# Optimization experiments

Hardware: AMD Instinct MI355X
Metric: run time of the kernel (lower is better)

## Reference

```python
import jax, jax.numpy as jnp
import numpy as np

V, D, OUT, H, FF, L, K, POOL = 4097, 128, 64, 8, 256, 2, 9, 20
B, LE, LP = 32, 3000, 2000
GRID, WIDTH = 5, 257
DR = OUT // 8  # channel-attention reduction


def _ln(x, p):
    mu = jnp.mean(x, -1, keepdims=True)
    var = jnp.mean((x - mu) ** 2, -1, keepdims=True)
    return (x - mu) * jax.lax.rsqrt(var + 1e-5) * p[0] + p[1]


def _rope(x):
    # x: [B,H,S,hd], interleaved rotary embedding
    S, hd = x.shape[-2], x.shape[-1]
    inv = 1.0 / (10000.0 ** (jnp.arange(0, hd, 2, dtype=jnp.float32) / hd))
    ang = jnp.arange(S, dtype=jnp.float32)[:, None] * inv[None, :]  # [S,hd/2]
    c, s = jnp.cos(ang), jnp.sin(ang)
    x1, x2 = x[..., 0::2], x[..., 1::2]
    return jnp.stack([x1 * c - x2 * s, x1 * s + x2 * c], axis=-1).reshape(x.shape)


def _cbat_layer(x, qkv_w, qkv_b, o_w, o_b, ca_w1, ca_w2, sa_w,
                ff1_w, ff1_b, ff2_w, ff2_b, ln1, ln2):
    # x: [B,S,d] (batch-first inside CBAT, matching x.permute(1,0,2) in torch)
    Bx, S, d = x.shape
    hd = d // H

    def proj(i):
        return (x @ qkv_w[i] + qkv_b[i]).reshape(Bx, S, H, hd).transpose(0, 2, 1, 3)

    q, k, v = proj(0), proj(1), proj(2)
    q, k = _rope(q), _rope(k)
    attn = jax.nn.softmax(jnp.einsum('bhqd,bhkd->bhqk', q, k) / jnp.sqrt(jnp.float32(hd)), axis=-1)
    ctx = jnp.einsum('bhqk,bhkd->bhqd', attn, v).transpose(0, 2, 1, 3).reshape(Bx, S, d)
    # CBAM-style channel attention (pool over sequence)
    avg, mx = ctx.mean(1), ctx.max(1)  # [B,d]
    ca = jax.nn.sigmoid(jax.nn.relu(avg @ ca_w1) @ ca_w2 + jax.nn.relu(mx @ ca_w1) @ ca_w2)
    ctx = ctx * ca[:, None, :]
    # CBAM-style spatial attention (pool over channels, conv over sequence)
    feat = jnp.stack([ctx.mean(-1), ctx.max(-1)], axis=1)  # [B,2,S]
    sa = jax.nn.sigmoid(jax.lax.conv_general_dilated(
        feat, sa_w[None], (1,), 'SAME', dimension_numbers=('NCH', 'OIH', 'NCH')))  # [B,1,S]
    ctx = ctx * sa.transpose(0, 2, 1)
    out = ctx @ o_w + o_b
    aloss = jnp.mean(attn ** 2)  # adaptive attention regularizer
    x = _ln(x + out, ln1)
    ff = jax.nn.relu(x @ ff1_w + ff1_b) @ ff2_w + ff2_b
    x = _ln(x + ff, ln2)
    return x, aloss


def _mha(q_in, k_in, v_in, in_w, in_b, out_w, out_b):
    # torch nn.MultiheadAttention math (batch-first layout here; math identical)
    d = q_in.shape[-1]
    hd = d // H
    Wq, Wk, Wv = jnp.split(in_w, 3, 0)
    bq, bk, bv = jnp.split(in_b, 3, 0)

    def heads(t):
        return t.reshape(t.shape[0], t.shape[1], H, hd).transpose(0, 2, 1, 3)

    q, k, v = heads(q_in @ Wq.T + bq), heads(k_in @ Wk.T + bk), heads(v_in @ Wv.T + bv)
    attn = jax.nn.softmax(jnp.einsum('bhqd,bhkd->bhqk', q, k) / jnp.sqrt(jnp.float32(hd)), axis=-1)
    ctx = jnp.einsum('bhqk,bhkd->bhqd', attn, v).transpose(0, 2, 1, 3).reshape(q_in.shape)
    return ctx @ out_w.T + out_b


def _fourier(x, wc, ws, b):
    # FourierKAN layer: sum_k a*cos(kx) + b*sin(kx)
    kx = x[:, :, None] * jnp.arange(1, GRID + 1, dtype=x.dtype)  # [B,in,g]
    return jnp.einsum('big,oig->bo', jnp.cos(kx), wc) + jnp.einsum('big,oig->bo', jnp.sin(kx), ws) + b


def _frontend(ids, emb, conv_w, conv_b, bn):
    x = emb[ids]  # [B,Lseq,D]
    x = jax.lax.conv_general_dilated(x.transpose(0, 2, 1), conv_w, (1,), 'VALID',
                                     dimension_numbers=('NCH', 'OIH', 'NCH')) + conv_b[None, :, None]
    x = jax.nn.relu(x)
    x = jax.lax.reduce_window(x, -jnp.inf, jax.lax.max, (1, 1, POOL), (1, 1, POOL), 'VALID')
    g, be, mu, var = bn[0], bn[1], bn[2], bn[3]  # BatchNorm1d (eval mode)
    x = (x - mu[None, :, None]) * jax.lax.rsqrt(var[None, :, None] + 1e-5) * g[None, :, None] + be[None, :, None]
    return x.transpose(0, 2, 1)  # [B,S,OUT]


def _forward(enhancer_ids, promoter_ids, emb_en, emb_pr, conv_w_en, conv_b_en, conv_w_pr, conv_b_pr,
             bn_en, bn_pr, t_qkv_w, t_qkv_b, t_o_w, t_o_b, t_ca_w1, t_ca_w2, t_sa_w,
             t_ff1_w, t_ff1_b, t_ff2_w, t_ff2_b, t_ln1, t_ln2,
             cross_in_w, cross_in_b, cross_out_w, cross_out_b,
             self_in_w, self_in_b, self_out_w, self_out_b,
             fk1_c, fk1_s, fk1_b, fk2_c, fk2_s, fk2_b):
    en = _frontend(enhancer_ids, emb_en, conv_w_en, conv_b_en, bn_en)
    pr = _frontend(promoter_ids, emb_pr, conv_w_pr, conv_b_pr, bn_pr)
    total_aloss = jnp.float32(0.0)
    branches = [en, pr]
    for s in range(2):  # 0=enhancer stack, 1=promoter stack
        x = branches[s]
        for l in range(L):
            x, al = _cbat_layer(x, t_qkv_w[s, l], t_qkv_b[s, l], t_o_w[s, l], t_o_b[s, l],
                                t_ca_w1[s, l], t_ca_w2[s, l], t_sa_w[s, l],
                                t_ff1_w[s, l], t_ff1_b[s, l], t_ff2_w[s, l], t_ff2_b[s, l],
                                t_ln1[s, l], t_ln2[s, l])
            total_aloss = total_aloss + al
        branches[s] = x
    en, pr = branches
    en_att = _mha(en, pr, pr, cross_in_w, cross_in_b, cross_out_w, cross_out_b)
    en_fin = _mha(en_att, en_att, en_att, self_in_w, self_in_b, self_out_w, self_out_b)
    pr_fin = _mha(pr, pr, pr, self_in_w, self_in_b, self_out_w, self_out_b)
    combined = jnp.concatenate([en_fin.mean(1), pr_fin.mean(1)], axis=1)  # AdaptiveAvgPool1d(1)
    hidden = _fourier(combined, fk1_c, fk1_s, fk1_b)
    result = _fourier(hidden, fk2_c, fk2_s, fk2_b)
    return jax.nn.sigmoid(result), combined, total_aloss


def setup_inputs() -> dict:
    key = jax.random.key(0)
    ks = iter(jax.random.split(key, 64))

    def nrm(shape, sc=0.02):
        return jax.random.normal(next(ks), shape, jnp.float32) * sc

    ln_init = lambda: jnp.stack([jnp.ones((2, L, OUT)), jnp.zeros((2, L, OUT))], axis=2)
    inp = {
        'enhancer_ids': jax.random.randint(next(ks), (B, LE), 0, V),
        'promoter_ids': jax.random.randint(next(ks), (B, LP), 0, V),
        'enhancer_features': jax.random.normal(next(ks), (B, 10), jnp.float32),
        'promoter_features': jax.random.normal(next(ks), (B, 10), jnp.float32),
        'emb_en': nrm((V, D), 0.1), 'emb_pr': nrm((V, D), 0.1),
        'conv_w_en': nrm((OUT, D, K)), 'conv_b_en': jnp.zeros((OUT,)),
        'conv_w_pr': nrm((OUT, D, K)), 'conv_b_pr': jnp.zeros((OUT,)),
        'bn_en': jnp.stack([jnp.ones(OUT), jnp.zeros(OUT), jnp.zeros(OUT), jnp.ones(OUT)]),
        'bn_pr': jnp.stack([jnp.ones(OUT), jnp.zeros(OUT), jnp.zeros(OUT), jnp.ones(OUT)]),
        't_qkv_w': nrm((2, L, 3, OUT, OUT)), 't_qkv_b': jnp.zeros((2, L, 3, OUT)),
        't_o_w': nrm((2, L, OUT, OUT)), 't_o_b': jnp.zeros((2, L, OUT)),
        't_ca_w1': nrm((2, L, OUT, DR)), 't_ca_w2': nrm((2, L, DR, OUT)),
        't_sa_w': nrm((2, L, 2, 7)),
        't_ff1_w': nrm((2, L, OUT, FF)), 't_ff1_b': jnp.zeros((2, L, FF)),
        't_ff2_w': nrm((2, L, FF, OUT)), 't_ff2_b': jnp.zeros((2, L, OUT)),
        't_ln1': ln_init(), 't_ln2': ln_init(),
        'cross_in_w': nrm((3 * OUT, OUT)), 'cross_in_b': jnp.zeros((3 * OUT,)),
        'cross_out_w': nrm((OUT, OUT)), 'cross_out_b': jnp.zeros((OUT,)),
        'self_in_w': nrm((3 * OUT, OUT)), 'self_in_b': jnp.zeros((3 * OUT,)),
        'self_out_w': nrm((OUT, OUT)), 'self_out_b': jnp.zeros((OUT,)),
        'fk1_c': nrm((WIDTH, 2 * OUT, GRID), 0.1), 'fk1_s': nrm((WIDTH, 2 * OUT, GRID), 0.1),
        'fk1_b': jnp.zeros((WIDTH,)),
        'fk2_c': nrm((1, WIDTH, GRID), 0.1), 'fk2_s': nrm((1, WIDTH, GRID), 0.1),
        'fk2_b': jnp.zeros((1,)),
    }
    return inp


def reference(enhancer_ids, promoter_ids, enhancer_features, promoter_features,
              emb_en, emb_pr, conv_w_en, conv_b_en, conv_w_pr, conv_b_pr,
              bn_en, bn_pr, t_qkv_w, t_qkv_b, t_o_w, t_o_b, t_ca_w1, t_ca_w2, t_sa_w,
              t_ff1_w, t_ff1_b, t_ff2_w, t_ff2_b, t_ln1, t_ln2,
              cross_in_w, cross_in_b, cross_out_w, cross_out_b,
              self_in_w, self_in_b, self_out_w, self_out_b,
              fk1_c, fk1_s, fk1_b, fk2_c, fk2_s, fk2_b):
    # enhancer_features / promoter_features are accepted but unused by the original forward
    return _forward(enhancer_ids, promoter_ids, emb_en, emb_pr, conv_w_en, conv_b_en,
                    conv_w_pr, conv_b_pr, bn_en, bn_pr, t_qkv_w, t_qkv_b, t_o_w, t_o_b,
                    t_ca_w1, t_ca_w2, t_sa_w, t_ff1_w, t_ff1_b, t_ff2_w, t_ff2_b, t_ln1, t_ln2,
                    cross_in_w, cross_in_b, cross_out_w, cross_out_b,
                    self_in_w, self_in_b, self_out_w, self_out_b,
                    fk1_c, fk1_s, fk1_b, fk2_c, fk2_s, fk2_b)
```

## Files before the change

kernel.cpp:

```cpp
#include <hip/hip_runtime.h>
#include <math.h>

#define BB 32
#define SE 149
#define SP 99
#define LE_LEN 3000
#define LP_LEN 2000
#define VT 8
#define ROWS_EN (BB * SE)
#define ROWS_PR (BB * SP)
#define ROWS_ALL (ROWS_EN + ROWS_PR)

__device__ __forceinline__ void row_decode(int row, int& branch, int& b,
                                           int& s, int& S, int& lrow) {
  if (row < ROWS_EN) { branch = 0; S = SE; lrow = row; b = row / SE; s = row - b * SE; }
  else { branch = 1; S = SP; lrow = row - ROWS_EN; b = lrow / SP; s = lrow - b * SP; }
}

__global__ __launch_bounds__(256) void prep_kernel(
    const float* __restrict__ cw_en, const float* __restrict__ cw_pr,
    const float* __restrict__ cross_in, const float* __restrict__ cross_out,
    const float* __restrict__ self_in, const float* __restrict__ self_out,
    float* __restrict__ W2en, float* __restrict__ W2pr,
    float* __restrict__ Wt, float* __restrict__ Al) {
  int bb = blockIdx.x;
  if (bb == 0 && threadIdx.x == 0) Al[0] = 0.f;
  if (bb < 576) {
    const float* src = (bb < 288) ? cw_en : cw_pr;
    float* dst = (bb < 288) ? W2en : W2pr;
    int i = ((bb < 288) ? bb : bb - 288) * 256 + threadIdx.x;
    int oc = i / 1152, r = i % 1152, ic = r / 9, k = r % 9;
    dst[ic * 576 + k * 64 + oc] = src[i];
  } else {
    int m = bb - 576;
    const float* src = (m < 3) ? cross_in + m * 4096
                     : (m == 3) ? cross_out
                     : (m < 7) ? self_in + (m - 4) * 4096
                     : self_out;
    for (int i = threadIdx.x; i < 4096; i += 256) {
      int o = i >> 6, c = i & 63;
      Wt[m * 4096 + c * 64 + o] = src[i];
    }
  }
}

__global__ __launch_bounds__(192) void conv_table_kernel(
    const float* __restrict__ emb_en, const float* __restrict__ emb_pr,
    const float* __restrict__ W2en, const float* __restrict__ W2pr,
    float* __restrict__ Cen, float* __restrict__ Cpr) {
  int blk = blockIdx.x;
  int branch = (blk >= 513);
  const float* emb = branch ? emb_pr : emb_en;
  const float* W2 = branch ? W2pr : W2en;
  float* C = branch ? Cpr : Cen;
  int v0 = (branch ? blk - 513 : blk) * VT;
  __shared__ float e[VT][128];
  int t = threadIdx.x;
  int nv = 4097 - v0; if (nv > VT) nv = VT;
  for (int i = t; i < nv * 128; i += 192) e[i >> 7][i & 127] = emb[v0 * 128 + i];
  __syncthreads();
  float a0[VT], a1[VT], a2[VT];
#pragma unroll
  for (int v = 0; v < VT; ++v) { a0[v] = 0.f; a1[v] = 0.f; a2[v] = 0.f; }
  for (int ic = 0; ic < 128; ++ic) {
    float w0 = W2[ic * 576 + t];
    float w1 = W2[ic * 576 + t + 192];
    float w2 = W2[ic * 576 + t + 384];
#pragma unroll
    for (int v = 0; v < VT; ++v) {
      float ev = e[v][ic];
      a0[v] += ev * w0; a1[v] += ev * w1; a2[v] += ev * w2;
    }
  }
  for (int v = 0; v < nv; ++v) {
    C[(size_t)(v0 + v) * 576 + t] = a0[v];
    C[(size_t)(v0 + v) * 576 + t + 192] = a1[v];
    C[(size_t)(v0 + v) * 576 + t + 384] = a2[v];
  }
}

__global__ __launch_bounds__(256) void frontend_kernel(
    const int* __restrict__ en_ids, const int* __restrict__ pr_ids,
    const float* __restrict__ Cen, const float* __restrict__ Cpr,
    const float* __restrict__ cb_en, const float* __restrict__ cb_pr,
    const float* __restrict__ bn_en, const float* __restrict__ bn_pr,
    float* __restrict__ Xen, float* __restrict__ Xpr) {
  int t = threadIdx.x;
  int wid = t >> 6, oc = t & 63;
  int row = blockIdx.x * 4 + wid;
  int branch, b, s, S, lrow;
  row_decode(row, branch, b, s, S, lrow);
  const int* ids = branch ? pr_ids : en_ids;
  int Lin = branch ? LP_LEN : LE_LEN;
  const float* C = branch ? Cpr : Cen;
  const float* cb = branch ? cb_pr : cb_en;
  const float* bn = branch ? bn_pr : bn_en;
  float* X = branch ? Xpr : Xen;
  __shared__ int idl[4][28];
  if (oc < 28) idl[wid][oc] = ids[b * Lin + s * 20 + oc];
  __syncthreads();
  float bias = cb[oc];
  float m = -INFINITY;
  for (int p = 0; p < 20; ++p) {
    float acc = bias;
#pragma unroll
    for (int k = 0; k < 9; ++k) acc += C[idl[wid][p + k] * 576 + k * 64 + oc];
    acc = fmaxf(acc, 0.f);
    m = fmaxf(m, acc);
  }
  float g = bn[oc], be = bn[64 + oc], mu = bn[128 + oc], var = bn[192 + oc];
  X[(size_t)lrow * 64 + oc] = (m - mu) * rsqrtf(var + 1e-5f) * g + be;
}

__global__ __launch_bounds__(256) void qkv_rope_kernel(
    const float* __restrict__ Xen, const float* __restrict__ Xpr,
    const float* __restrict__ t_qkv_w, const float* __restrict__ t_qkv_b, int l,
    float* __restrict__ Q, float* __restrict__ K, float* __restrict__ V) {
  int t = threadIdx.x;
  int wid = t >> 6, oc = t & 63;
  int row = blockIdx.x * 4 + wid;
  int branch, b, s, S, lrow;
  row_decode(row, branch, b, s, S, lrow);
  const float* X = branch ? Xpr : Xen;
  int idx = branch * 2 + l;
  const float* W = t_qkv_w + (size_t)idx * 3 * 4096;
  const float* bias = t_qkv_b + idx * 192;
  __shared__ float xr[4][64], qs[4][64], ks[4][64];
  xr[wid][oc] = X[lrow * 64 + oc];
  __syncthreads();
  float q0 = bias[oc], k0 = bias[64 + oc], v0 = bias[128 + oc];
  float q1 = 0.f, k1 = 0.f, v1 = 0.f;
  for (int c = 0; c < 64; c += 2) {
    float xa = xr[wid][c], xb = xr[wid][c + 1];
    q0 += xa * W[c * 64 + oc];
    q1 += xb * W[(c + 1) * 64 + oc];
    k0 += xa * W[4096 + c * 64 + oc];
    k1 += xb * W[4096 + (c + 1) * 64 + oc];
    v0 += xa * W[8192 + c * 64 + oc];
    v1 += xb * W[8192 + (c + 1) * 64 + oc];
  }
  float q = q0 + q1, k = k0 + k1, v = v0 + v1;
  qs[wid][oc] = q; ks[wid][oc] = k;
  V[row * 64 + oc] = v;
  __syncthreads();
  int j = oc & 7;
  int p = j >> 1;
  float inv = powf(10000.f, -(float)p * 0.25f);
  float ang = (float)s * inv;
  float cc = cosf(ang), ss = sinf(ang);
  float qo, ko;
  if ((j & 1) == 0) {
    qo = qs[wid][oc] * cc - qs[wid][oc + 1] * ss;
    ko = ks[wid][oc] * cc - ks[wid][oc + 1] * ss;
  } else {
    qo = qs[wid][oc - 1] * ss + qs[wid][oc] * cc;
    ko = ks[wid][oc - 1] * ss + ks[wid][oc] * cc;
  }
  Q[row * 64 + oc] = qo;
  K[row * 64 + oc] = ko;
}

__global__ __launch_bounds__(256) void attn_kernel(
    const float* __restrict__ Q, const float* __restrict__ K,
    const float* __restrict__ V, float* __restrict__ ctx,
    int nblk0, int Sq0, int Sk0, int qb0, int kb0, float als0,
    int Sq1, int Sk1, int qb1, int kb1, float als1,
    float* __restrict__ aloss_acc) {
  int blk = blockIdx.x;
  int bh, Sq, Sk, qb, kb; float als;
  if (blk < nblk0) { bh = blk; Sq = Sq0; Sk = Sk0; qb = qb0; kb = kb0; als = als0; }
  else { bh = blk - nblk0; Sq = Sq1; Sk = Sk1; qb = qb1; kb = kb1; als = als1; }
  int b = bh >> 3, h = bh & 7;
  __shared__ float kk[160 * 8], vv[160 * 8];
  int t = threadIdx.x;
  for (int i = t; i < Sk * 8; i += 256) {
    int r = i >> 3, j = i & 7;
    kk[i] = K[(kb + b * Sk + r) * 64 + h * 8 + j];
    vv[i] = V[(kb + b * Sk + r) * 64 + h * 8 + j];
  }
  __syncthreads();
  float rowsum2 = 0.f;
  if (t < Sq) {
    float q[8];
#pragma unroll
    for (int j = 0; j < 8; ++j) q[j] = Q[(qb + b * Sq + t) * 64 + h * 8 + j];
    float m = -INFINITY, sum = 0.f, sum2 = 0.f, acc[8];
#pragma unroll
    for (int j = 0; j < 8; ++j) acc[j] = 0.f;
    const float sc = 0.35355339059327373f;
    for (int kki = 0; kki < Sk; ++kki) {
      float sdot = 0.f;
#pragma unroll
      for (int j = 0; j < 8; ++j) sdot += q[j] * kk[kki * 8 + j];
      sdot *= sc;
      if (sdot > m) {
        float f = expf(m - sdot);
        sum *= f; sum2 *= f * f;
#pragma unroll
        for (int j = 0; j < 8; ++j) acc[j] *= f;
        m = sdot;
      }
      float e = expf(sdot - m);
      sum += e; sum2 += e * e;
#pragma unroll
      for (int j = 0; j < 8; ++j) acc[j] += e * vv[kki * 8 + j];
    }
    float invs = 1.f / sum;
#pragma unroll
    for (int j = 0; j < 8; ++j)
      ctx[(qb + b * Sq + t) * 64 + h * 8 + j] = acc[j] * invs;
    rowsum2 = sum2 * invs * invs;
  }
  if (als != 0.f) {
    float wsum = rowsum2;
    for (int off = 32; off; off >>= 1) wsum += __shfl_down(wsum, off, 64);
    __shared__ float wred[4];
    if ((t & 63) == 0) wred[t >> 6] = wsum;
    __syncthreads();
    if (t == 0) {
      float tot = wred[0] + wred[1] + wred[2] + wred[3];
      atomicAdd(aloss_acc, tot * als);
    }
  }
}

__global__ __launch_bounds__(512) void ca_kernel(
    const float* __restrict__ ctx, const float* __restrict__ t_ca_w1,
    const float* __restrict__ t_ca_w2, int l, float* __restrict__ ca) {
  int bp = blockIdx.x;
  int branch = bp >> 5, b = bp & 31;
  int S = branch ? SP : SE;
  int base = branch ? ROWS_EN : 0;
  int idx = branch * 2 + l;
  const float* W1 = t_ca_w1 + idx * 512;
  const float* W2 = t_ca_w2 + idx * 512;
  int t = threadIdx.x;
  int c = t & 63, seg = t >> 6;
  float sum = 0.f, mx = -INFINITY;
  for (int s = seg; s < S; s += 8) {
    float v = ctx[(size_t)(base + b * S + s) * 64 + c];
    sum += v; mx = fmaxf(mx, v);
  }
  __shared__ float ssum[8][64], smx[8][64];
  ssum[seg][c] = sum; smx[seg][c] = mx;
  __syncthreads();
  __shared__ float avg_l[64], mx_l[64], ha[8], hm[8];
  if (t < 64) {
    float a = 0.f, m = -INFINITY;
#pragma unroll
    for (int g = 0; g < 8; ++g) { a += ssum[g][t]; m = fmaxf(m, smx[g][t]); }
    avg_l[t] = a / (float)S; mx_l[t] = m;
  }
  __syncthreads();
  if (t < 8) {
    float a = 0.f, m2 = 0.f;
    for (int i = 0; i < 64; ++i) {
      a += avg_l[i] * W1[i * 8 + t];
      m2 += mx_l[i] * W1[i * 8 + t];
    }
    ha[t] = fmaxf(a, 0.f); hm[t] = fmaxf(m2, 0.f);
  }
  __syncthreads();
  if (t < 64) {
    float o = 0.f;
#pragma unroll
    for (int j = 0; j < 8; ++j) o += (ha[j] + hm[j]) * W2[j * 64 + t];
    ca[bp * 64 + t] = 1.f / (1.f + expf(-o));
  }
}

__global__ __launch_bounds__(256) void feat_kernel(
    float* __restrict__ ctx, const float* __restrict__ ca,
    float* __restrict__ fmean, float* __restrict__ fmax) {
  int row = blockIdx.x * 4 + (threadIdx.x >> 6);
  int branch, b, s, S, lrow;
  row_decode(row, branch, b, s, S, lrow);
  int c = threadIdx.x & 63;
  float v = ctx[row * 64 + c] * ca[(branch * 32 + b) * 64 + c];
  ctx[row * 64 + c] = v;
  float sum = v, mx = v;
  for (int off = 32; off; off >>= 1) {
    sum += __shfl_xor(sum, off, 64);
    mx = fmaxf(mx, __shfl_xor(mx, off, 64));
  }
  if (c == 0) { fmean[row] = sum * (1.f / 64.f); fmax[row] = mx; }
}

__global__ __launch_bounds__(256) void tail_kernel(
    const float* __restrict__ ctx, const float* __restrict__ fmean,
    const float* __restrict__ fmax, const float* __restrict__ t_sa_w,
    const float* __restrict__ t_o_w, const float* __restrict__ t_o_b,
    const float* __restrict__ t_ln1, const float* __restrict__ t_ff1_w,
    const float* __restrict__ t_ff1_b, const float* __restrict__ t_ff2_w,
    const float* __restrict__ t_ff2_b, const float* __restrict__ t_ln2,
    int l, float* __restrict__ Xen, float* __restrict__ Xpr) {
  int t = threadIdx.x;
  int wid = t >> 6, lane = t & 63;
  int row = blockIdx.x * 4 + wid;
  int branch, b, s, S, lrow;
  row_decode(row, branch, b, s, S, lrow);
  int idx = branch * 2 + l;
  const float* sa_w = t_sa_w + idx * 14;
  float sa = 0.f;
  if (lane == 0) {
    for (int k = 0; k < 7; ++k) {
      int p = s + k - 3;
      if (p >= 0 && p < S)
        sa += fmean[row - s + p] * sa_w[k] + fmax[row - s + p] * sa_w[7 + k];
    }
    sa = 1.f / (1.f + expf(-sa));
  }
  sa = __shfl(sa, 0, 64);
  __shared__ float rowv[4][64], xr[4][64], h[4][256];
  rowv[wid][lane] = ctx[row * 64 + lane] * sa;
  __syncthreads();
  const float* o_w = t_o_w + (size_t)idx * 4096;
  float p0 = t_o_b[idx * 64 + lane], p1 = 0.f, p2 = 0.f, p3 = 0.f;
  for (int c = 0; c < 64; c += 4) {
    p0 += rowv[wid][c] * o_w[c * 64 + lane];
    p1 += rowv[wid][c + 1] * o_w[(c + 1) * 64 + lane];
    p2 += rowv[wid][c + 2] * o_w[(c + 2) * 64 + lane];
    p3 += rowv[wid][c + 3] * o_w[(c + 3) * 64 + lane];
  }
  float o = (p0 + p1) + (p2 + p3);
  float* X = branch ? Xpr : Xen;
  float r = X[lrow * 64 + lane] + o;
  float mu = r;
  for (int of = 32; of; of >>= 1) mu += __shfl_xor(mu, of, 64);
  mu *= (1.f / 64.f);
  float d = r - mu;
  float var = d * d;
  for (int of = 32; of; of >>= 1) var += __shfl_xor(var, of, 64);
  var *= (1.f / 64.f);
  const float* ln1 = t_ln1 + idx * 128;
  float x1 = d * rsqrtf(var + 1e-5f) * ln1[lane] + ln1[64 + lane];
  xr[wid][lane] = x1;
  __syncthreads();
  const float* W1 = t_ff1_w + (size_t)idx * 16384;
  float a0 = t_ff1_b[idx * 256 + t], a1 = a0, a2 = a0, a3 = a0;
  for (int c = 0; c < 64; ++c) {
    float w = W1[c * 256 + t];
    a0 += xr[0][c] * w; a1 += xr[1][c] * w; a2 += xr[2][c] * w; a3 += xr[3][c] * w;
  }
  h[0][t] = fmaxf(a0, 0.f); h[1][t] = fmaxf(a1, 0.f);
  h[2][t] = fmaxf(a2, 0.f); h[3][t] = fmaxf(a3, 0.f);
  __syncthreads();
  const float* W2 = t_ff2_w + (size_t)idx * 16384;
  float q0 = t_ff2_b[idx * 64 + lane], q1 = 0.f, q2 = 0.f, q3 = 0.f;
  for (int j = 0; j < 256; j += 4) {
    q0 += h[wid][j] * W2[j * 64 + lane];
    q1 += h[wid][j + 1] * W2[(j + 1) * 64 + lane];
    q2 += h[wid][j + 2] * W2[(j + 2) * 64 + lane];
    q3 += h[wid][j + 3] * W2[(j + 3) * 64 + lane];
  }
  float o2 = (q0 + q1) + (q2 + q3);
  float r2 = x1 + o2;
  mu = r2;
  for (int of = 32; of; of >>= 1) mu += __shfl_xor(mu, of, 64);
  mu *= (1.f / 64.f);
  d = r2 - mu;
  var = d * d;
  for (int of = 32; of; of >>= 1) var += __shfl_xor(var, of, 64);
  var *= (1.f / 64.f);
  const float* ln2 = t_ln2 + idx * 128;
  X[lrow * 64 + lane] = d * rsqrtf(var + 1e-5f) * ln2[lane] + ln2[64 + lane];
}

__global__ __launch_bounds__(256) void cross_proj_kernel(
    const float* __restrict__ Xen, const float* __restrict__ Xpr,
    const float* __restrict__ Wt, const float* __restrict__ bias,
    float* __restrict__ Q, float* __restrict__ K, float* __restrict__ V) {
  int t = threadIdx.x;
  int wid = t >> 6, oc = t & 63;
  int blk = blockIdx.x;
  __shared__ float xr[4][64];
  if (blk < ROWS_EN / 4) {
    int row = blk * 4 + wid;
    xr[wid][oc] = Xen[row * 64 + oc];
    __syncthreads();
    float p0 = bias[oc], p1 = 0.f, p2 = 0.f, p3 = 0.f;
    for (int c = 0; c < 64; c += 4) {
      p0 += xr[wid][c] * Wt[c * 64 + oc];
      p1 += xr[wid][c + 1] * Wt[(c + 1) * 64 + oc];
      p2 += xr[wid][c + 2] * Wt[(c + 2) * 64 + oc];
      p3 += xr[wid][c + 3] * Wt[(c + 3) * 64 + oc];
    }
    Q[row * 64 + oc] = (p0 + p1) + (p2 + p3);
  } else {
    int lr = (blk - ROWS_EN / 4) * 4 + wid;
    xr[wid][oc] = Xpr[lr * 64 + oc];
    __syncthreads();
    float k0 = bias[64 + oc], k1 = 0.f, v0 = bias[128 + oc], v1 = 0.f;
    for (int c = 0; c < 64; c += 2) {
      float xa = xr[wid][c], xb = xr[wid][c + 1];
      k0 += xa * Wt[4096 + c * 64 + oc];
      k1 += xb * Wt[4096 + (c + 1) * 64 + oc];
      v0 += xa * Wt[8192 + c * 64 + oc];
      v1 += xb * Wt[8192 + (c + 1) * 64 + oc];
    }
    K[(ROWS_EN + lr) * 64 + oc] = k0 + k1;
    V[(ROWS_EN + lr) * 64 + oc] = v0 + v1;
  }
}

__global__ __launch_bounds__(256) void self_qkv_kernel(
    const float* __restrict__ inEn, const float* __restrict__ inPr,
    const float* __restrict__ Wt, const float* __restrict__ bias,
    float* __restrict__ Q, float* __restrict__ K, float* __restrict__ V) {
  int t = threadIdx.x;
  int wid = t >> 6, oc = t & 63;
  int row = blockIdx.x * 4 + wid;
  const float* in; int lrow;
  if (row < ROWS_EN) { in = inEn; lrow = row; }
  else { in = inPr; lrow = row - ROWS_EN; }
  __shared__ float xr[4][64];
  xr[wid][oc] = in[lrow * 64 + oc];
  __syncthreads();
  float q0 = bias[oc], k0 = bias[64 + oc], v0 = bias[128 + oc];
  float q1 = 0.f, k1 = 0.f, v1 = 0.f;
  for (int c = 0; c < 64; c += 2) {
    float xa = xr[wid][c], xb = xr[wid][c + 1];
    q0 += xa * Wt[c * 64 + oc];
    q1 += xb * Wt[(c + 1) * 64 + oc];
    k0 += xa * Wt[4096 + c * 64 + oc];
    k1 += xb * Wt[4096 + (c + 1) * 64 + oc];
    v0 += xa * Wt[8192 + c * 64 + oc];
    v1 += xb * Wt[8192 + (c + 1) * 64 + oc];
  }
  Q[row * 64 + oc] = q0 + q1;
  K[row * 64 + oc] = k0 + k1;
  V[row * 64 + oc] = v0 + v1;
}

__global__ __launch_bounds__(256) void dual_proj_kernel(
    const float* __restrict__ in, const float* __restrict__ Wt,
    const float* __restrict__ bias, float* __restrict__ out0,
    float* __restrict__ out1) {
  int t = threadIdx.x;
  int wid = t >> 6, oc = t & 63;
  int row = blockIdx.x * 4 + wid;
  float* out; int lrow;
  if (row < ROWS_EN) { out = out0; lrow = row; }
  else { out = out1; lrow = row - ROWS_EN; }
  __shared__ float xr[4][64];
  xr[wid][oc] = in[row * 64 + oc];
  __syncthreads();
  float p0 = bias[oc], p1 = 0.f, p2 = 0.f, p3 = 0.f;
  for (int c = 0; c < 64; c += 4) {
    p0 += xr[wid][c] * Wt[c * 64 + oc];
    p1 += xr[wid][c + 1] * Wt[(c + 1) * 64 + oc];
    p2 += xr[wid][c + 2] * Wt[(c + 2) * 64 + oc];
    p3 += xr[wid][c + 3] * Wt[(c + 3) * 64 + oc];
  }
  out[lrow * 64 + oc] = (p0 + p1) + (p2 + p3);
}

__global__ __launch_bounds__(512) void mean_trig_kernel(
    const float* __restrict__ en_fin, const float* __restrict__ pr_fin,
    float* __restrict__ comb, float* __restrict__ trig) {
  int b = blockIdx.x;
  int t = threadIdx.x;
  int col = t & 127, seg = t >> 7;
  float sum = 0.f;
  if (col < 64) {
    for (int s = seg; s < SE; s += 4) sum += en_fin[(b * SE + s) * 64 + col];
  } else {
    int c = col - 64;
    for (int s = seg; s < SP; s += 4) sum += pr_fin[(b * SP + s) * 64 + c];
  }
  __shared__ float red[4][128];
  __shared__ float comb_s[128];
  red[seg][col] = sum;
  __syncthreads();
  if (t < 128) {
    float tot = red[0][t] + red[1][t] + red[2][t] + red[3][t];
    float cv = tot / (t < 64 ? (float)SE : (float)SP);
    comb_s[t] = cv;
    comb[b * 128 + t] = cv;
  }
  __syncthreads();
  for (int i = t; i < 640; i += 512) {
    int ii = i / 5, g = i - ii * 5;
    float x = comb_s[ii] * (float)(g + 1);
    trig[b * 1280 + i] = cosf(x);
    trig[b * 1280 + 640 + i] = sinf(x);
  }
}

__global__ __launch_bounds__(256) void fourier1_kernel(
    const float* __restrict__ trig, const float* __restrict__ wc,
    const float* __restrict__ ws, const float* __restrict__ bias,
    float* __restrict__ hidden) {
  int b = blockIdx.x;
  int t = threadIdx.x;
  int wid = t >> 6, lane = t & 63;
  int o = blockIdx.y * 4 + wid;
  if (o >= 257) return;
  const float* ct = trig + b * 1280;
  const float* st = ct + 640;
  float acc = 0.f;
  for (int i = lane; i < 640; i += 64)
    acc += ct[i] * wc[(size_t)o * 640 + i] + st[i] * ws[(size_t)o * 640 + i];
  for (int off = 32; off; off >>= 1) acc += __shfl_xor(acc, off, 64);
  if (lane == 0) hidden[b * 257 + o] = acc + bias[o];
}

__global__ void fourier2_kernel(const float* __restrict__ hidden,
                                const float* __restrict__ wc,
                                const float* __restrict__ ws,
                                const float* __restrict__ bias,
                                const float* __restrict__ aloss_acc,
                                float* __restrict__ out) {
  int b = blockIdx.x;
  int t = threadIdx.x;
  float acc = 0.f;
  if (t < 257) {
    float x = hidden[b * 257 + t];
#pragma unroll
    for (int g = 0; g < 5; ++g) {
      float a = x * (float)(g + 1);
      acc += cosf(a) * wc[t * 5 + g] + sinf(a) * ws[t * 5 + g];
    }
  }
  for (int off = 32; off; off >>= 1) acc += __shfl_xor(acc, off, 64);
  __shared__ float wred[5];
  if ((t & 63) == 0) wred[t >> 6] = acc;
  __syncthreads();
  if (t == 0) {
    float tot = wred[0] + wred[1] + wred[2] + wred[3] + wred[4] + bias[0];
    out[b] = 1.f / (1.f + expf(-tot));
    if (b == 0) out[4128] = aloss_acc[0];
  }
}

extern "C" void kernel_launch(void* const* d_in, const int* in_sizes, int n_in,
                              void* d_out, int out_size, void* d_ws, size_t ws_size,
                              hipStream_t stream) {
  const int* en_ids = (const int*)d_in[0];
  const int* pr_ids = (const int*)d_in[1];
  const float* emb_en = (const float*)d_in[4];
  const float* emb_pr = (const float*)d_in[5];
  const float* conv_w_en = (const float*)d_in[6];
  const float* conv_b_en = (const float*)d_in[7];
  const float* conv_w_pr = (const float*)d_in[8];
  const float* conv_b_pr = (const float*)d_in[9];
  const float* bn_en = (const float*)d_in[10];
  const float* bn_pr = (const float*)d_in[11];
  const float* t_qkv_w = (const float*)d_in[12];
  const float* t_qkv_b = (const float*)d_in[13];
  const float* t_o_w = (const float*)d_in[14];
  const float* t_o_b = (const float*)d_in[15];
  const float* t_ca_w1 = (const float*)d_in[16];
  const float* t_ca_w2 = (const float*)d_in[17];
  const float* t_sa_w = (const float*)d_in[18];
  const float* t_ff1_w = (const float*)d_in[19];
  const float* t_ff1_b = (const float*)d_in[20];
  const float* t_ff2_w = (const float*)d_in[21];
  const float* t_ff2_b = (const float*)d_in[22];
  const float* t_ln1 = (const float*)d_in[23];
  const float* t_ln2 = (const float*)d_in[24];
  const float* cross_in_w = (const float*)d_in[25];
  const float* cross_in_b = (const float*)d_in[26];
  const float* cross_out_w = (const float*)d_in[27];
  const float* cross_out_b = (const float*)d_in[28];
  const float* self_in_w = (const float*)d_in[29];
  const float* self_in_b = (const float*)d_in[30];
  const float* self_out_w = (const float*)d_in[31];
  const float* self_out_b = (const float*)d_in[32];
  const float* fk1_c = (const float*)d_in[33];
  const float* fk1_s = (const float*)d_in[34];
  const float* fk1_b = (const float*)d_in[35];
  const float* fk2_c = (const float*)d_in[36];
  const float* fk2_s = (const float*)d_in[37];
  const float* fk2_b = (const float*)d_in[38];

  float* out = (float*)d_out;
  float* ws = (float*)d_ws;
  size_t off = 0;
  float* Cen = ws + off;  off += (size_t)4097 * 576;
  float* Cpr = ws + off;  off += (size_t)4097 * 576;
  float* W2en = ws + off; off += 73728;
  float* W2pr = ws + off; off += 73728;
  float* Wt = ws + off;   off += 8 * 4096;
  float* Xen = ws + off;  off += (size_t)ROWS_EN * 64;
  float* Xpr = ws + off;  off += (size_t)ROWS_PR * 64;
  float* Qb = ws + off;   off += (size_t)ROWS_ALL * 64;
  float* Kb = ws + off;   off += (size_t)ROWS_ALL * 64;
  float* Vb = ws + off;   off += (size_t)ROWS_ALL * 64;
  float* Ctx = ws + off;  off += (size_t)ROWS_ALL * 64;
  float* AttEn = ws + off; off += (size_t)ROWS_EN * 64;
  float* PrFin = ws + off; off += (size_t)ROWS_PR * 64;
  float* Fm = ws + off;   off += ROWS_ALL;
  float* Fx = ws + off;   off += ROWS_ALL;
  float* CaB = ws + off;  off += 2 * BB * 64;
  float* Hid = ws + off;  off += BB * 257;
  float* Trig = ws + off; off += (size_t)BB * 1280;
  float* Al = ws + off;   off += 8;

  const float als_en = 1.f / ((float)BB * 8.f * (float)SE * (float)SE);
  const float als_pr = 1.f / ((float)BB * 8.f * (float)SP * (float)SP);

  prep_kernel<<<584, 256, 0, stream>>>(conv_w_en, conv_w_pr, cross_in_w,
                                       cross_out_w, self_in_w, self_out_w,
                                       W2en, W2pr, Wt, Al);
  conv_table_kernel<<<1026, 192, 0, stream>>>(emb_en, emb_pr, W2en, W2pr, Cen, Cpr);
  frontend_kernel<<<ROWS_ALL / 4, 256, 0, stream>>>(en_ids, pr_ids, Cen, Cpr,
                                                    conv_b_en, conv_b_pr, bn_en,
                                                    bn_pr, Xen, Xpr);

  for (int l = 0; l < 2; ++l) {
    qkv_rope_kernel<<<ROWS_ALL / 4, 256, 0, stream>>>(Xen, Xpr, t_qkv_w,
                                                      t_qkv_b, l, Qb, Kb, Vb);
    attn_kernel<<<512, 256, 0, stream>>>(Qb, Kb, Vb, Ctx,
                                         256, SE, SE, 0, 0, als_en,
                                         SP, SP, ROWS_EN, ROWS_EN, als_pr, Al);
    ca_kernel<<<64, 512, 0, stream>>>(Ctx, t_ca_w1, t_ca_w2, l, CaB);
    feat_kernel<<<ROWS_ALL / 4, 256, 0, stream>>>(Ctx, CaB, Fm, Fx);
    tail_kernel<<<ROWS_ALL / 4, 256, 0, stream>>>(
        Ctx, Fm, Fx, t_sa_w, t_o_w, t_o_b, t_ln1, t_ff1_w, t_ff1_b,
        t_ff2_w, t_ff2_b, t_ln2, l, Xen, Xpr);
  }

  cross_proj_kernel<<<ROWS_ALL / 4, 256, 0, stream>>>(Xen, Xpr, Wt,
                                                      cross_in_b, Qb, Kb, Vb);
  attn_kernel<<<256, 256, 0, stream>>>(Qb, Kb, Vb, Ctx,
                                       256, SE, SP, 0, ROWS_EN, 0.f,
                                       0, 0, 0, 0, 0.f, Al);
  dual_proj_kernel<<<ROWS_EN / 4, 256, 0, stream>>>(Ctx, Wt + 3 * 4096,
                                                    cross_out_b, AttEn, AttEn);

  self_qkv_kernel<<<ROWS_ALL / 4, 256, 0, stream>>>(AttEn, Xpr, Wt + 4 * 4096,
                                                    self_in_b, Qb, Kb, Vb);
  attn_kernel<<<512, 256, 0, stream>>>(Qb, Kb, Vb, Ctx,
                                       256, SE, SE, 0, 0, 0.f,
                                       SP, SP, ROWS_EN, ROWS_EN, 0.f, Al);
  dual_proj_kernel<<<ROWS_ALL / 4, 256, 0, stream>>>(Ctx, Wt + 7 * 4096,
                                                     self_out_b, Xen, PrFin);

  mean_trig_kernel<<<BB, 512, 0, stream>>>(Xen, PrFin, out + 32, Trig);
  fourier1_kernel<<<dim3(BB, 65), 256, 0, stream>>>(Trig, fk1_c, fk1_s,
                                                    fk1_b, Hid);
  fourier2_kernel<<<BB, 320, 0, stream>>>(Hid, fk2_c, fk2_s, fk2_b, Al, out);
}
```

Baseline: 360.9 us.

## Split attention key range across two thread groups and merge partial softmax

The attention kernel now runs 384 threads as two groups of 192. Each group handles half of the key sequence for the same query rows, and the two online-softmax partial states (max, sum, sum of squares, accumulator) are merged through shared memory. This halves the serial key loop per thread and raises active threads per block. The exact expf is also replaced with the faster __expf intrinsic. The cost is extra shared memory, a second barrier, merge arithmetic, and slightly lower exp accuracy.

After: 325.3 us. -9.9%, faster.

```diff
diff --git a/kernel.cpp b/kernel.cpp
--- a/kernel.cpp
+++ b/kernel.cpp
@@ -160,7 +160,7 @@
   K[row * 64 + oc] = ko;
 }
 
-__global__ __launch_bounds__(256) void attn_kernel(
+__global__ __launch_bounds__(384) void attn_kernel(
     const float* __restrict__ Q, const float* __restrict__ K,
     const float* __restrict__ V, float* __restrict__ ctx,
     int nblk0, int Sq0, int Sk0, int qb0, int kb0, float als0,
@@ -172,53 +172,72 @@
   else { bh = blk - nblk0; Sq = Sq1; Sk = Sk1; qb = qb1; kb = kb1; als = als1; }
   int b = bh >> 3, h = bh & 7;
   __shared__ float kk[160 * 8], vv[160 * 8];
-  int t = threadIdx.x;
-  for (int i = t; i < Sk * 8; i += 256) {
+  __shared__ float pm[192], psum[192], psum2[192], pacc[192][8];
+  int t = threadIdx.x;
+  int g = t / 192, tq = t - g * 192;
+  for (int i = t; i < Sk * 8; i += 384) {
     int r = i >> 3, j = i & 7;
-    kk[i] = K[(kb + b * Sk + r) * 64 + h * 8 + j];
-    vv[i] = V[(kb + b * Sk + r) * 64 + h * 8 + j];
-  }
-  __syncthreads();
-  float rowsum2 = 0.f;
-  if (t < Sq) {
+    kk[i] = K[(size_t)(kb + b * Sk + r) * 64 + h * 8 + j];
+    vv[i] = V[(size_t)(kb + b * Sk + r) * 64 + h * 8 + j];
+  }
+  __syncthreads();
+  int half = (Sk + 1) >> 1;
+  int kbeg = g ? half : 0;
+  int kend = g ? Sk : half;
+  float m = -INFINITY, sum = 0.f, sum2 = 0.f, acc[8];
+#pragma unroll
+  for (int j = 0; j < 8; ++j) acc[j] = 0.f;
+  if (tq < Sq) {
     float q[8];
 #pragma unroll
-    for (int j = 0; j < 8; ++j) q[j] = Q[(qb + b * Sq + t) * 64 + h * 8 + j];
-    float m = -INFINITY, sum = 0.f, sum2 = 0.f, acc[8];
-#pragma unroll
-    for (int j = 0; j < 8; ++j) acc[j] = 0.f;
+    for (int j = 0; j < 8; ++j) q[j] = Q[(size_t)(qb + b * Sq + tq) * 64 + h * 8 + j];
     const float sc = 0.35355339059327373f;
-    for (int kki = 0; kki < Sk; ++kki) {
+    for (int kki = kbeg; kki < kend; ++kki) {
       float sdot = 0.f;
 #pragma unroll
       for (int j = 0; j < 8; ++j) sdot += q[j] * kk[kki * 8 + j];
       sdot *= sc;
       if (sdot > m) {
-        float f = expf(m - sdot);
+        float f = __expf(m - sdot);
         sum *= f; sum2 *= f * f;
 #pragma unroll
         for (int j = 0; j < 8; ++j) acc[j] *= f;
         m = sdot;
       }
-      float e = expf(sdot - m);
+      float e = __expf(sdot - m);
       sum += e; sum2 += e * e;
 #pragma unroll
       for (int j = 0; j < 8; ++j) acc[j] += e * vv[kki * 8 + j];
     }
-    float invs = 1.f / sum;
-#pragma unroll
-    for (int j = 0; j < 8; ++j)
-      ctx[(qb + b * Sq + t) * 64 + h * 8 + j] = acc[j] * invs;
-    rowsum2 = sum2 * invs * invs;
+  }
+  if (g == 1 && tq < Sq) {
+    pm[tq] = m; psum[tq] = sum; psum2[tq] = sum2;
+#pragma unroll
+    for (int j = 0; j < 8; ++j) pacc[tq][j] = acc[j];
+  }
+  __syncthreads();
+  float rowsum2 = 0.f;
+  if (g == 0 && tq < Sq) {
+    float m1 = pm[tq];
+    float mf = fmaxf(m, m1);
+    float f0 = __expf(m - mf), f1 = __expf(m1 - mf);
+    float sumf = sum * f0 + psum[tq] * f1;
+    float invs = 1.f / sumf;
+#pragma unroll
+    for (int j = 0; j < 8; ++j) {
+      float a = acc[j] * f0 + pacc[tq][j] * f1;
+      ctx[(size_t)(qb + b * Sq + tq) * 64 + h * 8 + j] = a * invs;
+    }
+    rowsum2 = (sum2 * f0 * f0 + psum2[tq] * f1 * f1) * invs * invs;
   }
   if (als != 0.f) {
     float wsum = rowsum2;
     for (int off = 32; off; off >>= 1) wsum += __shfl_down(wsum, off, 64);
-    __shared__ float wred[4];
+    __shared__ float wred[6];
     if ((t & 63) == 0) wred[t >> 6] = wsum;
     __syncthreads();
     if (t == 0) {
-      float tot = wred[0] + wred[1] + wred[2] + wred[3];
+      float tot = wred[0] + wred[1] + wred[2] + wred[3] + wred[4] + wred[5];
       atomicAdd(aloss_acc, tot * als);
     }
   }
@@ -611,7 +630,7 @@
   for (int l = 0; l < 2; ++l) {
     qkv_rope_kernel<<<ROWS_ALL / 4, 256, 0, stream>>>(Xen, Xpr, t_qkv_w,
                                                       t_qkv_b, l, Qb, Kb, Vb);
-    attn_kernel<<<512, 256, 0, stream>>>(Qb, Kb, Vb, Ctx,
+    attn_kernel<<<512, 384, 0, stream>>>(Qb, Kb, Vb, Ctx,
                                          256, SE, SE, 0, 0, als_en,
                                          SP, SP, ROWS_EN, ROWS_EN, als_pr, Al);
     ca_kernel<<<64, 512, 0, stream>>>(Ctx, t_ca_w1, t_ca_w2, l, CaB);
@@ -623,7 +642,7 @@
 
   cross_proj_kernel<<<ROWS_ALL / 4, 256, 0, stream>>>(Xen, Xpr, Wt,
                                                       cross_in_b, Qb, Kb, Vb);
-  attn_kernel<<<256, 256, 0, stream>>>(Qb, Kb, Vb, Ctx,
+  attn_kernel<<<256, 384, 0, stream>>>(Qb, Kb, Vb, Ctx,
                                        256, SE, SP, 0, ROWS_EN, 0.f,
                                        0, 0, 0, 0, 0.f, Al);
   dual_proj_kernel<<<ROWS_EN / 4, 256, 0, stream>>>(Ctx, Wt + 3 * 4096,
@@ -631,7 +650,7 @@
 
   self_qkv_kernel<<<ROWS_ALL / 4, 256, 0, stream>>>(AttEn, Xpr, Wt + 4 * 4096,
                                                     self_in_b, Qb, Kb, Vb);
-  attn_kernel<<<512, 256, 0, stream>>>(Qb, Kb, Vb, Ctx,
+  attn_kernel<<<512, 384, 0, stream>>>(Qb, Kb, Vb, Ctx,
                                        256, SE, SE, 0, 0, 0.f,
                                        SP, SP, ROWS_EN, ROWS_EN, 0.f, Al);
   dual_proj_kernel<<<ROWS_ALL / 4, 256, 0, stream>>>(Ctx, Wt + 7 * 4096,
```
